# Kernel optimization log

Measured on AMD Instinct MI355X. Metric: run time of the kernel, lower is better.

The kernel has to match this reference:

```python
import jax, jax.numpy as jnp
import numpy as np

N_NODES = 100000
N_EDGES = 1200000
D_IN = 64
D_HID = 64


def _gcn_layer(h_in, W, b, src, dst, norm, n_nodes):
    # h_in: [N, d_in]; W: [d_in, d_out]; norm: [E_total] symmetric deg norm
    h = h_in @ W                                  # [N, d_out]
    msg = h[src] * norm[:, None]                  # gather + scale, [E_total, d_out]
    agg = jax.ops.segment_sum(msg, dst, num_segments=n_nodes)  # scatter-add
    return agg + b


def _prelu(x, a):
    # per-channel PReLU: a broadcasts over nodes
    return jnp.where(x >= 0, x, a * x)


def setup_inputs() -> dict:
    key = jax.random.key(0)
    ks = jax.random.split(key, 8)
    x = jax.random.normal(ks[0], (N_NODES, D_IN), dtype=jnp.float32)
    edge_index = jax.random.randint(ks[1], (2, N_EDGES), 0, N_NODES, dtype=jnp.int64)
    # Glorot-ish weights, PyG GCNConv defaults: weight + bias; PReLU init slope 0.25
    W1 = jax.random.normal(ks[2], (D_IN, D_HID), dtype=jnp.float32) / np.sqrt(D_IN)
    b1 = jnp.zeros((D_HID,), dtype=jnp.float32)
    a1 = jnp.full((D_HID,), 0.25, dtype=jnp.float32)
    W2 = jax.random.normal(ks[3], (D_HID, D_HID), dtype=jnp.float32) / np.sqrt(D_HID)
    b2 = jnp.zeros((D_HID,), dtype=jnp.float32)
    a2 = jnp.full((D_HID,), 0.25, dtype=jnp.float32)
    return {"x": x, "edge_index": edge_index, "W1": W1, "b1": b1, "a1": a1,
            "W2": W2, "b2": b2, "a2": a2}


def reference(x, edge_index, W1, b1, a1, W2, b2, a2):
    n = x.shape[0]
    # add self-loops (GCNConv default add_self_loops=True)
    loops = jnp.arange(n, dtype=edge_index.dtype)
    src = jnp.concatenate([edge_index[0], loops])
    dst = jnp.concatenate([edge_index[1], loops])
    # symmetric normalization: deg computed on destination with unit edge weights
    deg = jax.ops.segment_sum(jnp.ones_like(src, dtype=x.dtype), dst, num_segments=n)
    dinv = jnp.where(deg > 0, jax.lax.rsqrt(deg), 0.0)
    norm = dinv[src] * dinv[dst]                  # [E + N]

    h = _gcn_layer(x, W1, b1, src, dst, norm, n)
    h = _prelu(h, a1)
    h = _gcn_layer(h, W2, b2, src, dst, norm, n)
    h = _prelu(h, a2)
    return h
```

## Files before the change

kernel.cpp:

```cpp
#include <hip/hip_runtime.h>
#include <hip/hip_bf16.h>
#include <hip/hip_fp16.h>

#define D 64
#define NB 256
#define BSHIFT 8
#define NBK 512
#define SUBS 8
#define SCAP 1024
#define CHUNK 8192
#define AGN 32
#define BFSTRIDE 16

typedef _Float16 f16x8 __attribute__((ext_vector_type(8)));
typedef float    f32x4 __attribute__((ext_vector_type(4)));


__global__ void __launch_bounds__(256, 4)
k_bin_gemm(const int* __restrict__ src, const int* __restrict__ dst,
           unsigned* __restrict__ records, int* __restrict__ bucket_fill,
           int E, int nbin,
           const float* __restrict__ X, const float* __restrict__ W,
           __half* __restrict__ H, int n, int ntiles, int gemmb) {
    __shared__ int cnt[NBK];
    __shared__ int gbase[NBK];
    const int t = threadIdx.x;

    if ((int)blockIdx.x < nbin) {
        const int slot = blockIdx.x & (SUBS - 1);
        cnt[t] = 0; cnt[t + 256] = 0;
        __syncthreads();

        const int base_e = blockIdx.x * CHUNK;
        unsigned rec[32];
        unsigned br[32];
#pragma unroll
        for (int i = 0; i < 8; ++i) {
            const int e0 = base_e + i * 1024 + t * 4;
            if (e0 + 3 < E) {
                int4 s4 = *reinterpret_cast<const int4*>(src + e0);
                int4 d4 = *reinterpret_cast<const int4*>(dst + e0);
                int ss[4] = {s4.x, s4.y, s4.z, s4.w};
                int dd[4] = {d4.x, d4.y, d4.z, d4.w};
#pragma unroll
                for (int j = 0; j < 4; ++j) {
                    int bk = dd[j] >> BSHIFT;
                    rec[i * 4 + j] = ((unsigned)ss[j] << BSHIFT) | (unsigned)(dd[j] & (NB - 1));
                    int rank = atomicAdd(&cnt[bk], 1);
                    br[i * 4 + j] = ((unsigned)bk << 16) | (unsigned)rank;
                }
            } else {
#pragma unroll
                for (int j = 0; j < 4; ++j) {
                    int e = e0 + j;
                    if (e < E) {
                        int s = src[e], d = dst[e];
                        int bk = d >> BSHIFT;
                        rec[i * 4 + j] = ((unsigned)s << BSHIFT) | (unsigned)(d & (NB - 1));
                        int rank = atomicAdd(&cnt[bk], 1);
                        br[i * 4 + j] = ((unsigned)bk << 16) | (unsigned)rank;
                    } else {
                        br[i * 4 + j] = 0xFFFFFFFFu;
                    }
                }
            }
        }
        __syncthreads();
#pragma unroll
        for (int rep = 0; rep < NBK / 256; ++rep) {
            int bk = t + rep * 256;
            if (cnt[bk] > 0)
                gbase[bk] = atomicAdd(&bucket_fill[(bk * SUBS + slot) * BFSTRIDE], cnt[bk]);
        }
        __syncthreads();
#pragma unroll
        for (int i = 0; i < 32; ++i) {
            if (br[i] != 0xFFFFFFFFu) {
                int bk = br[i] >> 16;
                int idx = gbase[bk] + (int)(br[i] & 0xFFFF);
                if (idx < SCAP)
                    records[((size_t)bk * SUBS + slot) * SCAP + idx] = rec[i];
            }
        }
    } else {
        const int lane = t & 63;
        const int wv   = t >> 6;
        const int r16  = lane & 15;
        const int g4   = lane >> 4;

        f16x8 Bh[4][2], Bl[4][2];
#pragma unroll
        for (int ct = 0; ct < 4; ++ct)
#pragma unroll
            for (int kt = 0; kt < 2; ++kt)
#pragma unroll
                for (int j = 0; j < 8; ++j) {
                    float w = W[(kt * 32 + g4 * 8 + j) * D + ct * 16 + r16];
                    _Float16 h = (_Float16)w;
                    Bh[ct][kt][j] = h;
                    Bl[ct][kt][j] = (_Float16)(w - (float)h);
                }

        const int gw = (blockIdx.x - nbin) * 4 + wv;
        for (int tile = gw; tile < ntiles; tile += gemmb * 4) {
            const int nb16 = tile * 16;
            int row = nb16 + r16;
            if (row > n - 1) row = n - 1;
            const float* xp = X + (size_t)row * D + g4 * 8;
            float4 x0 = *reinterpret_cast<const float4*>(xp);
            float4 x1 = *reinterpret_cast<const float4*>(xp + 4);
            float4 x2 = *reinterpret_cast<const float4*>(xp + 32);
            float4 x3 = *reinterpret_cast<const float4*>(xp + 36);
            float xs[16] = {x0.x, x0.y, x0.z, x0.w, x1.x, x1.y, x1.z, x1.w,
                            x2.x, x2.y, x2.z, x2.w, x3.x, x3.y, x3.z, x3.w};
            f16x8 Ah[2], Al[2];
#pragma unroll
            for (int kt = 0; kt < 2; ++kt)
#pragma unroll
                for (int j = 0; j < 8; ++j) {
                    float v = xs[kt * 8 + j];
                    _Float16 h = (_Float16)v;
                    Ah[kt][j] = h;
                    Al[kt][j] = (_Float16)(v - (float)h);
                }

            f32x4 acc[4];
#pragma unroll
            for (int ct = 0; ct < 4; ++ct)
                acc[ct] = (f32x4){0.f, 0.f, 0.f, 0.f};
#pragma unroll
            for (int ct = 0; ct < 4; ++ct) {
#pragma unroll
                for (int kt = 0; kt < 2; ++kt) {
                    acc[ct] = __builtin_amdgcn_mfma_f32_16x16x32_f16(Ah[kt], Bh[ct][kt], acc[ct], 0, 0, 0);
                    acc[ct] = __builtin_amdgcn_mfma_f32_16x16x32_f16(Al[kt], Bh[ct][kt], acc[ct], 0, 0, 0);
                    acc[ct] = __builtin_amdgcn_mfma_f32_16x16x32_f16(Ah[kt], Bl[ct][kt], acc[ct], 0, 0, 0);
                }
            }
#pragma unroll
            for (int ct = 0; ct < 4; ++ct)
#pragma unroll
                for (int r = 0; r < 4; ++r) {
                    int node = nb16 + g4 * 4 + r;
                    if (node < n)
                        H[(size_t)node * D + ct * 16 + r16] = __float2half_rn(acc[ct][r]);
                }
        }
    }
}


__global__ void k_csr(const unsigned* __restrict__ records,
                      const int* __restrict__ bucket_fill,
                      int* __restrict__ edge_base,
                      int* __restrict__ rowbeg, int* __restrict__ rowcnt,
                      float* __restrict__ dinv,
                      int* __restrict__ csr_src, __half* __restrict__ H, int n) {
    __shared__ int cnt[NB];
    __shared__ int excl[NB];
    __shared__ float ddi[NB];
    __shared__ int wsum[4];
    __shared__ int sbase;
    __shared__ int stage[SUBS * SCAP];

    const int t = threadIdx.x;
    const int b = blockIdx.x;
    const int lane = t & 63;

    int subcnt[SUBS];
    int cnt_e = 0;
#pragma unroll
    for (int s = 0; s < SUBS; ++s) {
        subcnt[s] = bucket_fill[(b * SUBS + s) * BFSTRIDE];
        cnt_e += subcnt[s];
    }

    cnt[t] = 0;
    __syncthreads();
#pragma unroll
    for (int s = 0; s < SUBS; ++s) {
        const size_t so = ((size_t)b * SUBS + s) * SCAP;
        for (int i = t; i < subcnt[s]; i += 256)
            atomicAdd(&cnt[records[so + i] & (NB - 1)], 1);
    }
    __syncthreads();

    const int c0 = cnt[t];
    int v = c0;
#pragma unroll
    for (int off = 1; off < 64; off <<= 1) {
        int u = __shfl_up(v, off, 64);
        if (lane >= off) v += u;
    }
    if (lane == 63) wsum[t >> 6] = v;
    if (t == 0) sbase = atomicAdd(edge_base, cnt_e);
    __syncthreads();
    int pre = 0;
#pragma unroll
    for (int w = 0; w < 4; ++w)
        if (w < (t >> 6)) pre += wsum[w];
    const int ex = v + pre - c0;
    excl[t] = ex;
    const int base = sbase;
    float di = rsqrtf((float)(c0 + 1));
    ddi[t] = di;
    {
        int node = b * NB + t;
        if (node < n) {
            rowbeg[node] = base + ex;
            rowcnt[node] = c0;
            dinv[node]   = di;
        }
    }
    cnt[t] = 0;
    __syncthreads();

#pragma unroll
    for (int s = 0; s < SUBS; ++s) {
        const size_t so = ((size_t)b * SUBS + s) * SCAP;
        for (int i = t; i < subcnt[s]; i += 256) {
            unsigned r = records[so + i];
            int d8 = r & (NB - 1);
            int rank = atomicAdd(&cnt[d8], 1);
            stage[excl[d8] + rank] = (int)(r >> BSHIFT);
        }
    }
    __syncthreads();

    for (int i = t; i < cnt_e; i += 256)
        csr_src[base + i] = stage[i];

#pragma unroll
    for (int r = 0; r < (NB * 8) / 256; ++r) {
        int idx = r * 256 + t;
        int nl = idx >> 3;
        int node = b * NB + nl;
        if (node < n) {
            int part = (idx & 7) * 8;
            uint4 g = *reinterpret_cast<uint4*>(H + (size_t)node * D + part);
            __half2* p = reinterpret_cast<__half2*>(&g);
            float s = ddi[nl];
#pragma unroll
            for (int i = 0; i < 4; ++i) {
                float2 f = __half22float2(p[i]);
                p[i] = __floats2half2_rn(f.x * s, f.y * s);
            }
            *reinterpret_cast<uint4*>(H + (size_t)node * D + part) = g;
        }
    }
}

__device__ __forceinline__ void edge_accum(const __half* __restrict__ Hn,
                                           const int* __restrict__ csr_src,
                                           int beg, int end, int part, float acc[8]) {
    int idx[8];
#pragma unroll
    for (int j = 0; j < 8; ++j)
        idx[j] = (beg + j < end) ? csr_src[beg + j] : 0;
    int k = beg;
    while (k < end) {
        int s[8];
        float w[8];
#pragma unroll
        for (int j = 0; j < 8; ++j) {
            s[j] = idx[j];
            w[j] = (k + j < end) ? 1.f : 0.f;
        }
        int kn = k + 8;
#pragma unroll
        for (int j = 0; j < 8; ++j)
            idx[j] = (kn + j < end) ? csr_src[kn + j] : 0;
        uint4 g[8];
#pragma unroll
        for (int j = 0; j < 8; ++j)
            g[j] = *reinterpret_cast<const uint4*>(Hn + (size_t)s[j] * D + part);
#pragma unroll
        for (int j = 0; j < 8; ++j) {
            const __half2* p = reinterpret_cast<const __half2*>(&g[j]);
#pragma unroll
            for (int i = 0; i < 4; ++i) {
                float2 f = __half22float2(p[i]);
                acc[2 * i + 0] += w[j] * f.x;
                acc[2 * i + 1] += w[j] * f.y;
            }
        }
        k = kn;
    }
}


__global__ void __launch_bounds__(256, 4)
k_agg_gemm(const __half* __restrict__ Hn1,
           const int* __restrict__ rowbeg,
           const int* __restrict__ rowcnt,
           const int* __restrict__ csr_src,
           const float* __restrict__ dinv,
           const float* __restrict__ b1, const float* __restrict__ a1,
           const float* __restrict__ W2,
           __half* __restrict__ Hn2, int n) {
    __shared__ float Yl[AGN][68];
    __shared__ float Zl[AGN][68];

    const int t    = threadIdx.x;
    const int lane = t & 63;
    const int wv   = t >> 6;
    const int r16  = lane & 15;
    const int g4   = lane >> 4;
    const int rt   = wv >> 1;
    const int cp   = wv & 1;

    f16x8 Bh[2][2], Bl[2][2];
#pragma unroll
    for (int ci = 0; ci < 2; ++ci)
#pragma unroll
        for (int kt = 0; kt < 2; ++kt)
#pragma unroll
            for (int j = 0; j < 8; ++j) {
                float w = W2[(kt * 32 + g4 * 8 + j) * D + (cp * 2 + ci) * 16 + r16];
                _Float16 h = (_Float16)w;
                Bh[ci][kt][j] = h;
                Bl[ci][kt][j] = (_Float16)(w - (float)h);
            }

    const int nl   = t >> 3;
    const int part = (t & 7) * 8;
    const int node = blockIdx.x * AGN + nl;

    if (node < n) {
        float di = dinv[node];
        float acc[8];
        {
            uint4 g = *reinterpret_cast<const uint4*>(Hn1 + (size_t)node * D + part);
            const __half2* p = reinterpret_cast<const __half2*>(&g);
#pragma unroll
            for (int i = 0; i < 4; ++i) {
                float2 f = __half22float2(p[i]);
                acc[2 * i + 0] = f.x;
                acc[2 * i + 1] = f.y;
            }
        }
        const int beg = rowbeg[node];
        edge_accum(Hn1, csr_src, beg, beg + rowcnt[node], part, acc);

        const float4 b0 = *reinterpret_cast<const float4*>(b1 + part);
        const float4 b4 = *reinterpret_cast<const float4*>(b1 + part + 4);
        const float4 a0 = *reinterpret_cast<const float4*>(a1 + part);
        const float4 a4 = *reinterpret_cast<const float4*>(a1 + part + 4);
        float y0 = acc[0] * di + b0.x, y1 = acc[1] * di + b0.y;
        float y2 = acc[2] * di + b0.z, y3 = acc[3] * di + b0.w;
        float y4 = acc[4] * di + b4.x, y5 = acc[5] * di + b4.y;
        float y6 = acc[6] * di + b4.z, y7 = acc[7] * di + b4.w;
        Yl[nl][part + 0] = (y0 >= 0.f) ? y0 : a0.x * y0;
        Yl[nl][part + 1] = (y1 >= 0.f) ? y1 : a0.y * y1;
        Yl[nl][part + 2] = (y2 >= 0.f) ? y2 : a0.z * y2;
        Yl[nl][part + 3] = (y3 >= 0.f) ? y3 : a0.w * y3;
        Yl[nl][part + 4] = (y4 >= 0.f) ? y4 : a4.x * y4;
        Yl[nl][part + 5] = (y5 >= 0.f) ? y5 : a4.y * y5;
        Yl[nl][part + 6] = (y6 >= 0.f) ? y6 : a4.z * y6;
        Yl[nl][part + 7] = (y7 >= 0.f) ? y7 : a4.w * y7;
        if ((t & 7) == 0) Yl[nl][64] = di;
    }
    __syncthreads();

    {
        f32x4 acc2[2];
        acc2[0] = (f32x4){0.f, 0.f, 0.f, 0.f};
        acc2[1] = (f32x4){0.f, 0.f, 0.f, 0.f};
#pragma unroll
        for (int kt = 0; kt < 2; ++kt) {
            const float* yp = &Yl[rt * 16 + r16][kt * 32 + g4 * 8];
            f16x8 Ah, Al;
#pragma unroll
            for (int j = 0; j < 8; ++j) {
                float v = yp[j];
                _Float16 h = (_Float16)v;
                Ah[j] = h;
                Al[j] = (_Float16)(v - (float)h);
            }
#pragma unroll
            for (int ci = 0; ci < 2; ++ci) {
                acc2[ci] = __builtin_amdgcn_mfma_f32_16x16x32_f16(Ah, Bh[ci][kt], acc2[ci], 0, 0, 0);
                acc2[ci] = __builtin_amdgcn_mfma_f32_16x16x32_f16(Al, Bh[ci][kt], acc2[ci], 0, 0, 0);
                acc2[ci] = __builtin_amdgcn_mfma_f32_16x16x32_f16(Ah, Bl[ci][kt], acc2[ci], 0, 0, 0);
            }
        }
#pragma unroll
        for (int ci = 0; ci < 2; ++ci)
#pragma unroll
            for (int r = 0; r < 4; ++r) {
                int row = rt * 16 + g4 * 4 + r;
                float dr = Yl[row][64];
                Zl[row][(cp * 2 + ci) * 16 + r16] = acc2[ci][r] * dr;
            }
    }
    __syncthreads();

    if (node >= n) return;
    float4 z0 = *reinterpret_cast<const float4*>(&Zl[nl][part]);
    float4 z1 = *reinterpret_cast<const float4*>(&Zl[nl][part + 4]);
    __half2 h0 = __floats2half2_rn(z0.x, z0.y);
    __half2 h1 = __floats2half2_rn(z0.z, z0.w);
    __half2 h2 = __floats2half2_rn(z1.x, z1.y);
    __half2 h3 = __floats2half2_rn(z1.z, z1.w);
    uint4 pack;
    pack.x = *reinterpret_cast<unsigned int*>(&h0);
    pack.y = *reinterpret_cast<unsigned int*>(&h1);
    pack.z = *reinterpret_cast<unsigned int*>(&h2);
    pack.w = *reinterpret_cast<unsigned int*>(&h3);
    *reinterpret_cast<uint4*>(Hn2 + (size_t)node * D + part) = pack;
}


__global__ void k_aggregate(const __half* __restrict__ Hn,
                            const int* __restrict__ rowbeg,
                            const int* __restrict__ rowcnt,
                            const int* __restrict__ csr_src,
                            const float* __restrict__ dinv,
                            const float* __restrict__ b, const float* __restrict__ a,
                            float* __restrict__ out, int n) {
    int t = blockIdx.x * blockDim.x + threadIdx.x;
    int node = t >> 3;
    if (node >= n) return;
    int part = (t & 7) * 8;

    float di = dinv[node];
    float acc[8];
    {
        uint4 g = *reinterpret_cast<const uint4*>(Hn + (size_t)node * D + part);
        const __half2* p = reinterpret_cast<const __half2*>(&g);
#pragma unroll
        for (int i = 0; i < 4; ++i) {
            float2 f = __half22float2(p[i]);
            acc[2 * i + 0] = f.x;
            acc[2 * i + 1] = f.y;
        }
    }
    const int beg = rowbeg[node];
    edge_accum(Hn, csr_src, beg, beg + rowcnt[node], part, acc);

    const float4 b0 = *reinterpret_cast<const float4*>(b + part);
    const float4 b4 = *reinterpret_cast<const float4*>(b + part + 4);
    const float4 a0 = *reinterpret_cast<const float4*>(a + part);
    const float4 a4 = *reinterpret_cast<const float4*>(a + part + 4);
    float4 r0, r1;
    r0.x = acc[0] * di + b0.x; r0.y = acc[1] * di + b0.y;
    r0.z = acc[2] * di + b0.z; r0.w = acc[3] * di + b0.w;
    r1.x = acc[4] * di + b4.x; r1.y = acc[5] * di + b4.y;
    r1.z = acc[6] * di + b4.z; r1.w = acc[7] * di + b4.w;
    r0.x = (r0.x >= 0.f) ? r0.x : a0.x * r0.x;
    r0.y = (r0.y >= 0.f) ? r0.y : a0.y * r0.y;
    r0.z = (r0.z >= 0.f) ? r0.z : a0.z * r0.z;
    r0.w = (r0.w >= 0.f) ? r0.w : a0.w * r0.w;
    r1.x = (r1.x >= 0.f) ? r1.x : a4.x * r1.x;
    r1.y = (r1.y >= 0.f) ? r1.y : a4.y * r1.y;
    r1.z = (r1.z >= 0.f) ? r1.z : a4.z * r1.z;
    r1.w = (r1.w >= 0.f) ? r1.w : a4.w * r1.w;
    float* o = out + (size_t)node * D + part;
    *reinterpret_cast<float4*>(o) = r0;
    *reinterpret_cast<float4*>(o + 4) = r1;
}

extern "C" void kernel_launch(void* const* d_in, const int* in_sizes, int n_in,
                              void* d_out, int out_size, void* d_ws, size_t ws_size,
                              hipStream_t stream) {
    const float* x  = (const float*)d_in[0];
    const int*   ei = (const int*)  d_in[1];
    const float* W1 = (const float*)d_in[2];
    const float* b1 = (const float*)d_in[3];
    const float* a1 = (const float*)d_in[4];
    const float* W2 = (const float*)d_in[5];
    const float* b2 = (const float*)d_in[6];
    const float* a2 = (const float*)d_in[7];
    float* out = (float*)d_out;

    const int n   = in_sizes[0] / D;
    const int E   = in_sizes[1] / 2;
    const int n64 = n * D;

    const int* src = ei;
    const int* dst = ei + E;

    const int nbuckets = (n + NB - 1) >> BSHIFT;

    int*      bucket_fill = (int*)d_ws;
    int*      edge_base   = bucket_fill + 60000;
    unsigned* records     = (unsigned*)(bucket_fill + 4096 * BFSTRIDE);
    int*      rowbeg      = (int*)(records + (size_t)nbuckets * SUBS * SCAP);
    int*      rowcnt      = rowbeg + ((n + 256) & ~255);
    float*    dinv        = (float*)(rowcnt + ((n + 256) & ~255));
    int*      csr_src     = (int*)(dinv + ((n + 256) & ~255));
    __half*   Hn1         = (__half*)(csr_src + ((E + 255) & ~255));
    __half*   Hn2         = Hn1 + (((size_t)n64 + 256) & ~(size_t)255);

    const int B = 256;
    const int nbin   = (E + CHUNK - 1) / CHUNK;
    const int gemmb  = 877;
    const int ntiles = (n + 15) / 16;

    hipMemsetAsync(bucket_fill, 0, 4096 * BFSTRIDE * sizeof(int), stream);

    k_bin_gemm<<<nbin + gemmb, B, 0, stream>>>(src, dst, records, bucket_fill, E, nbin,
                                               x, W1, Hn1, n, ntiles, gemmb);
    k_csr<<<nbuckets, B, 0, stream>>>(records, bucket_fill, edge_base,
                                      rowbeg, rowcnt, dinv, csr_src, Hn1, n);
    k_agg_gemm<<<(n + AGN - 1) / AGN, B, 0, stream>>>(Hn1, rowbeg, rowcnt, csr_src, dinv,
                                                      b1, a1, W2, Hn2, n);
    k_aggregate<<<(n * 8 + B - 1) / B, B, 0, stream>>>(Hn2, rowbeg, rowcnt, csr_src, dinv,
                                                       b2, a2, out, n);
}
```

Measured before the change: 177.3 us.

## Build CSR via global degree count, block scan, and atomic fill

Replaces the two-level bucketed binning (shared-memory bucket records, then a per-bucket local sort into CSR) with three plain stages. Global atomics count destination degrees, a per-block scan with an atomic base assigns row starts, and a separate fill kernel scatters source ids using per-node atomic cursors. This removes the bounded bucket record buffers and the SCAP overflow clipping, but adds an extra kernel launch plus heavy global atomic traffic and uncoalesced scatter writes. Rows end up in non-deterministic order and are no longer sorted by any locality.

```diff
diff --git a/kernel.cpp b/kernel.cpp
--- a/kernel.cpp
+++ b/kernel.cpp
@@ -3,83 +3,30 @@
 #include <hip/hip_fp16.h>
 
 #define D 64
-#define NB 256
-#define BSHIFT 8
-#define NBK 512
-#define SUBS 8
-#define SCAP 1024
-#define CHUNK 8192
 #define AGN 32
-#define BFSTRIDE 16
 
 typedef _Float16 f16x8 __attribute__((ext_vector_type(8)));
 typedef float    f32x4 __attribute__((ext_vector_type(4)));
 
 
 __global__ void __launch_bounds__(256, 4)
-k_bin_gemm(const int* __restrict__ src, const int* __restrict__ dst,
-           unsigned* __restrict__ records, int* __restrict__ bucket_fill,
-           int E, int nbin,
-           const float* __restrict__ X, const float* __restrict__ W,
-           __half* __restrict__ H, int n, int ntiles, int gemmb) {
-    __shared__ int cnt[NBK];
-    __shared__ int gbase[NBK];
+k_count_gemm(const int* __restrict__ dst, int* __restrict__ deg,
+             int E, int cntb,
+             const float* __restrict__ X, const float* __restrict__ W,
+             __half* __restrict__ H, int n, int ntiles, int gemmb) {
     const int t = threadIdx.x;
 
-    if ((int)blockIdx.x < nbin) {
-        const int slot = blockIdx.x & (SUBS - 1);
-        cnt[t] = 0; cnt[t + 256] = 0;
-        __syncthreads();
-
-        const int base_e = blockIdx.x * CHUNK;
-        unsigned rec[32];
-        unsigned br[32];
-#pragma unroll
-        for (int i = 0; i < 8; ++i) {
-            const int e0 = base_e + i * 1024 + t * 4;
+    if ((int)blockIdx.x < cntb) {
+        for (int e0 = blockIdx.x * 1024 + t * 4; e0 < E; e0 += cntb * 1024) {
             if (e0 + 3 < E) {
-                int4 s4 = *reinterpret_cast<const int4*>(src + e0);
                 int4 d4 = *reinterpret_cast<const int4*>(dst + e0);
-                int ss[4] = {s4.x, s4.y, s4.z, s4.w};
-                int dd[4] = {d4.x, d4.y, d4.z, d4.w};
-#pragma unroll
-                for (int j = 0; j < 4; ++j) {
-                    int bk = dd[j] >> BSHIFT;
-                    rec[i * 4 + j] = ((unsigned)ss[j] << BSHIFT) | (unsigned)(dd[j] & (NB - 1));
-                    int rank = atomicAdd(&cnt[bk], 1);
-                    br[i * 4 + j] = ((unsigned)bk << 16) | (unsigned)rank;
-                }
+                atomicAdd(&deg[d4.x], 1);
+                atomicAdd(&deg[d4.y], 1);
+                atomicAdd(&deg[d4.z], 1);
+                atomicAdd(&deg[d4.w], 1);
             } else {
-#pragma unroll
-                for (int j = 0; j < 4; ++j) {
-                    int e = e0 + j;
-                    if (e < E) {
-                        int s = src[e], d = dst[e];
-                        int bk = d >> BSHIFT;
-                        rec[i * 4 + j] = ((unsigned)s << BSHIFT) | (unsigned)(d & (NB - 1));
-                        int rank = atomicAdd(&cnt[bk], 1);
-                        br[i * 4 + j] = ((unsigned)bk << 16) | (unsigned)rank;
-                    } else {
-                        br[i * 4 + j] = 0xFFFFFFFFu;
-                    }
-                }
-            }
-        }
-        __syncthreads();
-#pragma unroll
-        for (int rep = 0; rep < NBK / 256; ++rep) {
-            int bk = t + rep * 256;
-            if (cnt[bk] > 0)
-                gbase[bk] = atomicAdd(&bucket_fill[(bk * SUBS + slot) * BFSTRIDE], cnt[bk]);
-        }
-        __syncthreads();
-#pragma unroll
-        for (int i = 0; i < 32; ++i) {
-            if (br[i] != 0xFFFFFFFFu) {
-                int bk = br[i] >> 16;
-                int idx = gbase[bk] + (int)(br[i] & 0xFFFF);
-                if (idx < SCAP)
-                    records[((size_t)bk * SUBS + slot) * SCAP + idx] = rec[i];
+                for (int j = 0; j < 4; ++j)
+                    if (e0 + j < E) atomicAdd(&deg[dst[e0 + j]], 1);
             }
         }
     } else {
@@ -101,7 +48,7 @@
                     Bl[ct][kt][j] = (_Float16)(w - (float)h);
                 }
 
-        const int gw = (blockIdx.x - nbin) * 4 + wv;
+        const int gw = (blockIdx.x - cntb) * 4 + wv;
         for (int tile = gw; tile < ntiles; tile += gemmb * 4) {
             const int nb16 = tile * 16;
             int row = nb16 + r16;
@@ -150,42 +97,20 @@
 }
 
 
-__global__ void k_csr(const unsigned* __restrict__ records,
-                      const int* __restrict__ bucket_fill,
-                      int* __restrict__ edge_base,
-                      int* __restrict__ rowbeg, int* __restrict__ rowcnt,
-                      float* __restrict__ dinv,
-                      int* __restrict__ csr_src, __half* __restrict__ H, int n) {
-    __shared__ int cnt[NB];
-    __shared__ int excl[NB];
-    __shared__ float ddi[NB];
+__global__ void k_rowbeg(const int* __restrict__ deg,
+                         int* __restrict__ edge_base,
+                         int* __restrict__ rowbeg, int* __restrict__ fillpos,
+                         float* __restrict__ dinv, __half* __restrict__ H, int n) {
     __shared__ int wsum[4];
     __shared__ int sbase;
-    __shared__ int stage[SUBS * SCAP];
+    __shared__ float ddi[256];
 
     const int t = threadIdx.x;
     const int b = blockIdx.x;
     const int lane = t & 63;
-
-    int subcnt[SUBS];
-    int cnt_e = 0;
-#pragma unroll
-    for (int s = 0; s < SUBS; ++s) {
-        subcnt[s] = bucket_fill[(b * SUBS + s) * BFSTRIDE];
-        cnt_e += subcnt[s];
-    }
-
-    cnt[t] = 0;
-    __syncthreads();
-#pragma unroll
-    for (int s = 0; s < SUBS; ++s) {
-        const size_t so = ((size_t)b * SUBS + s) * SCAP;
-        for (int i = t; i < subcnt[s]; i += 256)
-            atomicAdd(&cnt[records[so + i] & (NB - 1)], 1);
-    }
-    __syncthreads();
-
-    const int c0 = cnt[t];
+    const int node = b * 256 + t;
+
+    const int c0 = (node < n) ? deg[node] : 0;
     int v = c0;
 #pragma unroll
     for (int off = 1; off < 64; off <<= 1) {
@@ -193,51 +118,31 @@
         if (lane >= off) v += u;
     }
     if (lane == 63) wsum[t >> 6] = v;
-    if (t == 0) sbase = atomicAdd(edge_base, cnt_e);
     __syncthreads();
     int pre = 0;
 #pragma unroll
     for (int w = 0; w < 4; ++w)
         if (w < (t >> 6)) pre += wsum[w];
-    const int ex = v + pre - c0;
-    excl[t] = ex;
-    const int base = sbase;
+    if (t == 255) sbase = atomicAdd(edge_base, v + pre);
+    __syncthreads();
+    const int ex = sbase + v + pre - c0;
     float di = rsqrtf((float)(c0 + 1));
     ddi[t] = di;
-    {
-        int node = b * NB + t;
-        if (node < n) {
-            rowbeg[node] = base + ex;
-            rowcnt[node] = c0;
-            dinv[node]   = di;
-        }
-    }
-    cnt[t] = 0;
+    if (node < n) {
+        rowbeg[node]  = ex;
+        fillpos[node] = ex;
+        dinv[node]    = di;
+    }
     __syncthreads();
 
 #pragma unroll
-    for (int s = 0; s < SUBS; ++s) {
-        const size_t so = ((size_t)b * SUBS + s) * SCAP;
-        for (int i = t; i < subcnt[s]; i += 256) {
-            unsigned r = records[so + i];
-            int d8 = r & (NB - 1);
-            int rank = atomicAdd(&cnt[d8], 1);
-            stage[excl[d8] + rank] = (int)(r >> BSHIFT);
-        }
-    }
-    __syncthreads();
-
-    for (int i = t; i < cnt_e; i += 256)
-        csr_src[base + i] = stage[i];
-
-#pragma unroll
-    for (int r = 0; r < (NB * 8) / 256; ++r) {
+    for (int r = 0; r < 8; ++r) {
         int idx = r * 256 + t;
         int nl = idx >> 3;
-        int node = b * NB + nl;
-        if (node < n) {
+        int nd = b * 256 + nl;
+        if (nd < n) {
             int part = (idx & 7) * 8;
-            uint4 g = *reinterpret_cast<uint4*>(H + (size_t)node * D + part);
+            uint4 g = *reinterpret_cast<uint4*>(H + (size_t)nd * D + part);
             __half2* p = reinterpret_cast<__half2*>(&g);
             float s = ddi[nl];
 #pragma unroll
@@ -245,7 +150,28 @@
                 float2 f = __half22float2(p[i]);
                 p[i] = __floats2half2_rn(f.x * s, f.y * s);
             }
-            *reinterpret_cast<uint4*>(H + (size_t)node * D + part) = g;
+            *reinterpret_cast<uint4*>(H + (size_t)nd * D + part) = g;
+        }
+    }
+}
+
+
+__global__ void k_fill(const int* __restrict__ src, const int* __restrict__ dst,
+                       int* __restrict__ fillpos, int* __restrict__ csr_src,
+                       int E, int fillb) {
+    const int t = threadIdx.x;
+    for (int e0 = blockIdx.x * 1024 + t * 4; e0 < E; e0 += fillb * 1024) {
+        if (e0 + 3 < E) {
+            int4 s4 = *reinterpret_cast<const int4*>(src + e0);
+            int4 d4 = *reinterpret_cast<const int4*>(dst + e0);
+            csr_src[atomicAdd(&fillpos[d4.x], 1)] = s4.x;
+            csr_src[atomicAdd(&fillpos[d4.y], 1)] = s4.y;
+            csr_src[atomicAdd(&fillpos[d4.z], 1)] = s4.z;
+            csr_src[atomicAdd(&fillpos[d4.w], 1)] = s4.w;
+        } else {
+            for (int j = 0; j < 4; ++j)
+                if (e0 + j < E)
+                    csr_src[atomicAdd(&fillpos[dst[e0 + j]], 1)] = src[e0 + j];
         }
     }
 }
@@ -476,35 +402,36 @@
     const int n   = in_sizes[0] / D;
     const int E   = in_sizes[1] / 2;
     const int n64 = n * D;
+    const int n_pad = (n + 255) & ~255;
+    const int E_pad = (E + 255) & ~255;
 
     const int* src = ei;
     const int* dst = ei + E;
 
-    const int nbuckets = (n + NB - 1) >> BSHIFT;
-
-    int*      bucket_fill = (int*)d_ws;
-    int*      edge_base   = bucket_fill + 60000;
-    unsigned* records     = (unsigned*)(bucket_fill + 4096 * BFSTRIDE);
-    int*      rowbeg      = (int*)(records + (size_t)nbuckets * SUBS * SCAP);
-    int*      rowcnt      = rowbeg + ((n + 256) & ~255);
-    float*    dinv        = (float*)(rowcnt + ((n + 256) & ~255));
-    int*      csr_src     = (int*)(dinv + ((n + 256) & ~255));
-    __half*   Hn1         = (__half*)(csr_src + ((E + 255) & ~255));
-    __half*   Hn2         = Hn1 + (((size_t)n64 + 256) & ~(size_t)255);
+    int*      deg       = (int*)d_ws;
+    int*      edge_base = deg + n_pad;
+    int*      rowbeg    = edge_base + 256;
+    int*      fillpos   = rowbeg + n_pad;
+    float*    dinv      = (float*)(fillpos + n_pad);
+    int*      csr_src   = (int*)(dinv + n_pad);
+    __half*   Hn1       = (__half*)(csr_src + E_pad);
+    __half*   Hn2       = Hn1 + (((size_t)n64 + 256) & ~(size_t)255);
 
     const int B = 256;
-    const int nbin   = (E + CHUNK - 1) / CHUNK;
-    const int gemmb  = 877;
+    const int cntb   = 256;
+    const int gemmb  = 768;
+    const int fillb  = 512;
     const int ntiles = (n + 15) / 16;
-
-    hipMemsetAsync(bucket_fill, 0, 4096 * BFSTRIDE * sizeof(int), stream);
-
-    k_bin_gemm<<<nbin + gemmb, B, 0, stream>>>(src, dst, records, bucket_fill, E, nbin,
-                                               x, W1, Hn1, n, ntiles, gemmb);
-    k_csr<<<nbuckets, B, 0, stream>>>(records, bucket_fill, edge_base,
-                                      rowbeg, rowcnt, dinv, csr_src, Hn1, n);
-    k_agg_gemm<<<(n + AGN - 1) / AGN, B, 0, stream>>>(Hn1, rowbeg, rowcnt, csr_src, dinv,
+    const int nscan  = (n + 255) >> 8;
+
+    hipMemsetAsync(deg, 0, (n_pad + 256) * sizeof(int), stream);
+
+    k_count_gemm<<<cntb + gemmb, B, 0, stream>>>(dst, deg, E, cntb,
+                                                 x, W1, Hn1, n, ntiles, gemmb);
+    k_rowbeg<<<nscan, B, 0, stream>>>(deg, edge_base, rowbeg, fillpos, dinv, Hn1, n);
+    k_fill<<<fillb, B, 0, stream>>>(src, dst, fillpos, csr_src, E, fillb);
+    k_agg_gemm<<<(n + AGN - 1) / AGN, B, 0, stream>>>(Hn1, rowbeg, deg, csr_src, dinv,
                                                       b1, a1, W2, Hn2, n);
-    k_aggregate<<<(n * 8 + B - 1) / B, B, 0, stream>>>(Hn2, rowbeg, rowcnt, csr_src, dinv,
+    k_aggregate<<<(n * 8 + B - 1) / B, B, 0, stream>>>(Hn2, rowbeg, deg, csr_src, dinv,
                                                        b2, a2, out, n);
 }
```

After: 287.6 us. 1.62x slower.
